# Kernel tuning notes

Measured on AMD Instinct MI355X. Metric: run time of the kernel, lower is better.

The kernel has to match this reference:

```python
import jax, jax.numpy as jnp
import numpy as np


def setup_inputs() -> dict:
    key = jax.random.key(0)
    ks = jax.random.split(key, 8)
    B, E, R, D, H = 8, 50000, 1000, 128, 256
    return {
        "head": jax.random.randint(ks[0], (B,), 0, E),
        "relation": jax.random.randint(ks[1], (B,), 0, R),
        "k": 10,
        "ent_emb": jax.random.normal(ks[2], (E, D), jnp.float32),
        "rel_emb": jax.random.normal(ks[3], (R, D), jnp.float32),
        "W1": jax.random.normal(ks[4], (3 * D, H), jnp.float32) * 0.05,
        "b1": jax.random.normal(ks[5], (H,), jnp.float32) * 0.05,
        "W2": jax.random.normal(ks[6], (H,), jnp.float32) * 0.05,
        "b2": jax.random.normal(ks[7], (1,), jnp.float32) * 0.05,
    }


def reference(head, relation, k, ent_emb, rel_emb, W1, b1, W2, b2):
    D = ent_emb.shape[1]
    # score_net first layer on cat([h, r, t]) == h@W1h + r@W1r + t@W1t (same math,
    # avoids materializing the [B*E, 3D] concat).
    W1h, W1r, W1t = W1[:D], W1[D:2 * D], W1[2 * D:]
    h = ent_emb[head]            # [B, D]
    r = rel_emb[relation]        # [B, D]
    ph = h @ W1h + r @ W1r + b1  # [B, H] -- head/relation part, computed once
    pt = ent_emb @ W1t           # [E, H] -- tail part over all entities
    hidden = jax.nn.relu(ph[:, None, :] + pt[None, :, :])   # [B, E, H]
    scores = jnp.einsum('beh,h->be', hidden, W2) + b2[0]     # [B, E]
    top_scores, top_indices = jax.lax.top_k(scores, k)
    return top_indices, top_scores
```

## Files before the change

kernel.cpp:

```cpp
#include <hip/hip_runtime.h>

#define D 128
#define HDIM 256
#define NB 8
#define NSHARD 32
#define CPS 16
#define LCPS 4
#define NCAND (NSHARD * CPS)
#define PHW 16
#define WPAD 136

typedef short bf16x8 __attribute__((ext_vector_type(8)));
typedef float f32x4 __attribute__((ext_vector_type(4)));

__device__ __forceinline__ unsigned short f2bf(float x) {
    unsigned u = __float_as_uint(x);
    unsigned r = u + 0x7FFF + ((u >> 16) & 1);
    return (unsigned short)(r >> 16);
}
__device__ __forceinline__ bf16x8 pack_bf8(float4 u, float4 v) {
    union { bf16x8 v8; unsigned short s[8]; } r;
    r.s[0] = f2bf(u.x); r.s[1] = f2bf(u.y); r.s[2] = f2bf(u.z); r.s[3] = f2bf(u.w);
    r.s[4] = f2bf(v.x); r.s[5] = f2bf(v.y); r.s[6] = f2bf(v.z); r.s[7] = f2bf(v.w);
    return r.v8;
}

__device__ __forceinline__ unsigned long long sk_encode(float v, int idx) {
    unsigned u = __float_as_uint(v);
    u = (u & 0x80000000u) ? ~u : (u | 0x80000000u);
    return ((unsigned long long)u << 32) | (unsigned)(0xFFFFFFFFu - (unsigned)idx);
}
__device__ __forceinline__ float sk_val(unsigned long long key) {
    const unsigned u = (unsigned)(key >> 32);
    return (u & 0x80000000u) ? __uint_as_float(u & 0x7FFFFFFFu) : __uint_as_float(~u);
}
__device__ __forceinline__ int sk_idx(unsigned long long key) {
    return (int)(0xFFFFFFFFu - (unsigned)(key & 0xFFFFFFFFu));
}
__device__ __forceinline__ unsigned long long wave_max64(unsigned long long m) {
#pragma unroll
    for (int s = 32; s > 0; s >>= 1) {
        const unsigned long long o = __shfl_xor(m, s, 64);
        if (o > m) m = o;
    }
    return m;
}

__global__ __launch_bounds__(1024) void prep_kernel(
        const int* __restrict__ head, const int* __restrict__ relation,
        const float* __restrict__ ent_emb, const float* __restrict__ rel_emb,
        const float* __restrict__ W1, const float* __restrict__ b1,
        const float* __restrict__ W2, float* __restrict__ phW,
        unsigned short* __restrict__ w1tt) {
    __shared__ float part[4][HDIM];
    const int w = blockIdx.x;
    const int tid = threadIdx.x;
    const int h = tid & 255;
    const int sl = tid >> 8;
    if (w < NB) {
        const int b = w;
        const long hidx = head[b];
        const long ridx = relation[b];
        const float* hrow = ent_emb + hidx * D;
        const float* rrow = rel_emb + ridx * D;
        float acc = 0.f;
        const int d0 = sl * 32;
#pragma unroll 8
        for (int dd = 0; dd < 32; ++dd) {
            const int d = d0 + dd;
            acc += hrow[d] * W1[d * HDIM + h];
            acc += rrow[d] * W1[(D + d) * HDIM + h];
        }
        part[sl][h] = acc;
        __syncthreads();
        if (sl == 0) {
            phW[h * PHW + b] = part[0][h] + part[1][h] + part[2][h] + part[3][h] + b1[h];
            if (b == 0) phW[h * PHW + 8] = W2[h];
        }
    } else {
        const int k0 = (w - NB) * 16 + sl * 4;
        const float* w1t = W1 + 2 * D * HDIM;
        unsigned short pk[4];
#pragma unroll
        for (int j = 0; j < 4; ++j)
            pk[j] = f2bf(w1t[(k0 + j) * HDIM + h]);
        *(ushort4*)(w1tt + h * D + k0) = make_ushort4(pk[0], pk[1], pk[2], pk[3]);
    }
}

__global__ __launch_bounds__(512, 2) void score_kernel(
        const float* __restrict__ ent_emb, const unsigned short* __restrict__ w1tt,
        const float* __restrict__ phW, float* __restrict__ scores, int E) {
    __shared__ __align__(16) unsigned short wL[HDIM][WPAD];
    __shared__ float phB[NB][HDIM];
    __shared__ float w2L[HDIM];

    const int tid = threadIdx.x;
    const int lane = tid & 63;
    const int wave = tid >> 6;
    const int lm = lane & 15;
    const int q = lane >> 4;
    const int base_e = blockIdx.x * 128 + wave * 16;

    const float* arow = ent_emb + (size_t)min(base_e + lm, E - 1) * D;
    bf16x8 aF[4];
#pragma unroll
    for (int kk = 0; kk < 4; ++kk) {
        const float4 u = *(const float4*)(arow + kk * 32 + q * 8);
        const float4 v = *(const float4*)(arow + kk * 32 + q * 8 + 4);
        aF[kk] = pack_bf8(u, v);
    }

#pragma unroll
    for (int i = 0; i < 8; ++i) {
        const int c = i * 512 + tid;
        const int row = c >> 4;
        const int col = (c & 15) << 3;
        *(uint4*)(&wL[row][col]) = *(const uint4*)(w1tt + row * D + col);
    }
    if (tid < HDIM) {
        const float4 p0 = *(const float4*)(phW + tid * PHW);
        const float4 p1 = *(const float4*)(phW + tid * PHW + 4);
        phB[0][tid] = -p0.x; phB[1][tid] = -p0.y; phB[2][tid] = -p0.z; phB[3][tid] = -p0.w;
        phB[4][tid] = -p1.x; phB[5][tid] = -p1.y; phB[6][tid] = -p1.z; phB[7][tid] = -p1.w;
        w2L[tid] = phW[tid * PHW + 8];
    }
    __syncthreads();

    float sp[NB * 4];
#pragma unroll
    for (int i = 0; i < NB * 4; ++i) sp[i] = 0.f;

#pragma unroll
    for (int t = 0; t < 16; ++t) {
        const int h = t * 16 + lm;
        bf16x8 bF[4];
#pragma unroll
        for (int kk = 0; kk < 4; ++kk)
            bF[kk] = *(const bf16x8*)(&wL[h][kk * 32 + q * 8]);

        float nphv[8];
#pragma unroll
        for (int b = 0; b < NB; ++b) nphv[b] = phB[b][h];
        const float w2v = w2L[h];

        f32x4 acc = (f32x4){0.f, 0.f, 0.f, 0.f};
#pragma unroll
        for (int kk = 0; kk < 4; ++kk)
            acc = __builtin_amdgcn_mfma_f32_16x16x32_bf16(aF[kk], bF[kk], acc, 0, 0, 0);

#pragma unroll
        for (int b = 0; b < NB; ++b)
#pragma unroll
            for (int r = 0; r < 4; ++r)
                sp[b * 4 + r] += fmaxf(acc[r], nphv[b]) * w2v;
    }

#pragma unroll
    for (int m = 1; m <= 8; m <<= 1) {
#pragma unroll
        for (int i = 0; i < NB * 4; ++i)
            sp[i] += __shfl_xor(sp[i], m, 64);
    }
    if (lm == 0) {
#pragma unroll
        for (int r = 0; r < 4; ++r) {
            const int e = base_e + q * 4 + r;
            if (e < E) {
#pragma unroll
                for (int b = 0; b < NB; ++b)
                    scores[(size_t)b * E + e] = sp[b * 4 + r];
            }
        }
    }
}

__global__ __launch_bounds__(512) void topk_rescore_kernel(
        const float* __restrict__ scores, int E,
        const float* __restrict__ ent_emb, const float* __restrict__ W1,
        const float* __restrict__ phW, const float* __restrict__ b2,
        unsigned long long* __restrict__ cand_exact) {
    const int b = blockIdx.x >> 5;
    const int s = blockIdx.x & 31;
    const int tid = threadIdx.x;
    const int lane = tid & 63;
    const int wave = tid >> 6;

    __shared__ unsigned long long cl[8 * CPS];
    __shared__ unsigned long long s2[32];
    __shared__ unsigned long long candk[CPS];
    __shared__ int eIdxs[CPS];
    __shared__ float entR[CPS][D];
    __shared__ float red[8][8];

    {
        const int shard = (E + NSHARD - 1) / NSHARD;
        const int start = s * shard;
        const int end = min(E, start + shard);
        const float* row = scores + (size_t)b * E;

        unsigned long long keys[LCPS];
#pragma unroll
        for (int i = 0; i < LCPS; ++i) keys[i] = 0ull;

        for (int e = start + tid; e < end; e += 512) {
            unsigned long long key = sk_encode(row[e], e);
            if (key > keys[LCPS - 1]) {
#pragma unroll
                for (int j = 0; j < LCPS; ++j) {
                    const bool gt = key > keys[j];
                    const unsigned long long mx = gt ? key : keys[j];
                    key = gt ? keys[j] : key;
                    keys[j] = mx;
                }
            }
        }
        for (int r = 0; r < CPS; ++r) {
            const unsigned long long m = wave_max64(keys[0]);
            if (keys[0] == m) {
#pragma unroll
                for (int j = 0; j < LCPS - 1; ++j) keys[j] = keys[j + 1];
                keys[LCPS - 1] = 0ull;
            }
            if (lane == 0) cl[wave * CPS + r] = m;
        }
        __syncthreads();
        if (wave < 2) {
            unsigned long long v = cl[wave * 64 + lane];
#pragma unroll
            for (int kk = 2; kk <= 64; kk <<= 1) {
#pragma unroll
                for (int j = kk >> 1; j > 0; j >>= 1) {
                    const unsigned long long o = __shfl_xor(v, j, 64);
                    const bool keep_min = (((lane & j) == 0) == ((lane & kk) != 0));
                    const unsigned long long mn = v < o ? v : o;
                    const unsigned long long mx = v < o ? o : v;
                    v = keep_min ? mn : mx;
                }
            }
            if (lane < 16) s2[wave * 16 + lane] = v;
        }
        __syncthreads();
        if (wave == 0) {
            unsigned long long v = 0ull;
            if (lane < 16) v = s2[lane];
            else if (lane < 32) v = s2[47 - lane];
#pragma unroll
            for (int j = 16; j > 0; j >>= 1) {
                const unsigned long long o = __shfl_xor(v, j, 64);
                const unsigned long long mn = v < o ? v : o;
                const unsigned long long mx = v < o ? o : v;
                v = ((lane & j) == 0) ? mx : mn;
            }
            if (lane < 16) candk[lane] = v;
        }
        __syncthreads();
    }

    if (tid < CPS) eIdxs[tid] = sk_idx(candk[tid]);
    __syncthreads();
    for (int t = tid; t < CPS * (D / 4); t += 512) {
        const int rowc = t >> 5, c4 = (t & 31) * 4;
        *(float4*)(&entR[rowc][c4]) =
            *(const float4*)(ent_emb + (size_t)eIdxs[rowc] * D + c4);
    }
    __syncthreads();

    const int h = tid & 255;
    const int chalf = tid >> 8;
    const float* w1t = W1 + 2 * D * HDIM;
    float acc[8];
#pragma unroll
    for (int c = 0; c < 8; ++c) acc[c] = 0.f;
    for (int d0 = 0; d0 < D; d0 += 4) {
        float w[4];
#pragma unroll
        for (int j = 0; j < 4; ++j) w[j] = w1t[(d0 + j) * HDIM + h];
#pragma unroll
        for (int c = 0; c < 8; ++c) {
            const float4 f = *(const float4*)(&entR[chalf * 8 + c][d0]);
            acc[c] += f.x * w[0] + f.y * w[1] + f.z * w[2] + f.w * w[3];
        }
    }
    const float phv = phW[h * PHW + b];
    const float w2v = phW[h * PHW + 8];
    float sc[8];
#pragma unroll
    for (int c = 0; c < 8; ++c) sc[c] = fmaxf(acc[c] + phv, 0.f) * w2v;

#pragma unroll
    for (int m = 1; m <= 32; m <<= 1)
#pragma unroll
        for (int c = 0; c < 8; ++c) sc[c] += __shfl_xor(sc[c], m, 64);
    if (lane == 0)
#pragma unroll
        for (int c = 0; c < 8; ++c) red[wave][c] = sc[c];
    __syncthreads();
    if (tid < CPS) {
        const int ch = tid >> 3, ci = tid & 7;
        const float v = red[ch * 4 + 0][ci] + red[ch * 4 + 1][ci] +
                        red[ch * 4 + 2][ci] + red[ch * 4 + 3][ci] + b2[0];
        cand_exact[(size_t)(b * NSHARD + s) * CPS + tid] = sk_encode(v, eIdxs[tid]);
    }
}

__global__ __launch_bounds__(64) void final_kernel(
        const unsigned long long* __restrict__ cand_exact, int k,
        float* __restrict__ out) {
    const int lane = threadIdx.x;
    const int b = blockIdx.x;
    unsigned long long lk[8];
#pragma unroll
    for (int j = 0; j < 8; ++j)
        lk[j] = cand_exact[(size_t)b * NCAND + j * 64 + lane];
#pragma unroll
    for (int i = 0; i < 7; ++i)
#pragma unroll
        for (int j = i + 1; j < 8; ++j)
            if (lk[i] < lk[j]) {
                const unsigned long long t = lk[i];
                lk[i] = lk[j];
                lk[j] = t;
            }
    for (int r = 0; r < k; ++r) {
        const unsigned long long m = wave_max64(lk[0]);
        if (lk[0] == m) {
#pragma unroll
            for (int j = 0; j < 7; ++j) lk[j] = lk[j + 1];
            lk[7] = 0ull;
        }
        if (lane == 0) {
            out[b * k + r] = (float)sk_idx(m);
            out[NB * k + b * k + r] = sk_val(m);
        }
    }
}

extern "C" void kernel_launch(void* const* d_in, const int* in_sizes, int n_in,
                              void* d_out, int out_size, void* d_ws, size_t ws_size,
                              hipStream_t stream) {
    const int*   head     = (const int*)d_in[0];
    const int*   relation = (const int*)d_in[1];
    const float* ent_emb  = (const float*)d_in[3];
    const float* rel_emb  = (const float*)d_in[4];
    const float* W1       = (const float*)d_in[5];
    const float* b1       = (const float*)d_in[6];
    const float* W2       = (const float*)d_in[7];
    const float* b2       = (const float*)d_in[8];

    const int B = in_sizes[0];
    const int E = in_sizes[3] / D;
    int k = out_size / (2 * B);
    if (k > CPS) k = CPS;

    char* ws = (char*)d_ws;
    unsigned long long* cand_exact = (unsigned long long*)ws;
    float*          phW       = (float*)(ws + 32768);
    unsigned short* w1tt      = (unsigned short*)(ws + 49152);
    float*          scores    = (float*)(ws + 114688);
    float*          out       = (float*)d_out;

    prep_kernel<<<NB + 8, 1024, 0, stream>>>(head, relation, ent_emb, rel_emb,
                                             W1, b1, W2, phW, w1tt);
    const int nblk = (E + 127) / 128;
    score_kernel<<<nblk, 512, 0, stream>>>(ent_emb, w1tt, phW, scores, E);
    topk_rescore_kernel<<<NB * NSHARD, 512, 0, stream>>>(
        scores, E, ent_emb, W1, phW, b2, cand_exact);
    final_kernel<<<NB, 64, 0, stream>>>(cand_exact, k, out);
}
```

Measured before the change: 133.1 us.

## Process two entity tiles per wave and use packed FMA epilogue in score kernel

The score kernel now runs 256 threads per block, with each wave handling 32 entities (two 16-row MFMA tiles) instead of 16. Each B fragment and phase value loaded from LDS is therefore reused across two tiles. The relu-times-W2 epilogue is rewritten with v_pk_fma_f32 and packed adds, and the per-h phase values and W2 are interleaved into one transposed LDS array so they load as vectors. This aims to cut LDS read traffic and VALU instruction count per entity, at the cost of more registers per thread and half as many threads per block.

After: 135.6 us. Within noise of the previous version (+1.9%).

```diff
diff --git a/kernel.cpp b/kernel.cpp
--- a/kernel.cpp
+++ b/kernel.cpp
@@ -9,9 +9,11 @@
 #define NCAND (NSHARD * CPS)
 #define PHW 16
 #define WPAD 136
+#define PHT 10
 
 typedef short bf16x8 __attribute__((ext_vector_type(8)));
 typedef float f32x4 __attribute__((ext_vector_type(4)));
+typedef float f32x2 __attribute__((ext_vector_type(2)));
 
 __device__ __forceinline__ unsigned short f2bf(float x) {
     unsigned u = __float_as_uint(x);
@@ -23,6 +25,16 @@
     r.s[0] = f2bf(u.x); r.s[1] = f2bf(u.y); r.s[2] = f2bf(u.z); r.s[3] = f2bf(u.w);
     r.s[4] = f2bf(v.x); r.s[5] = f2bf(v.y); r.s[6] = f2bf(v.z); r.s[7] = f2bf(v.w);
     return r.v8;
+}
+
+__device__ __forceinline__ f32x2 pk_fma(f32x2 a, f32x2 b, f32x2 c) {
+    asm("v_pk_fma_f32 %0, %1, %2, %0" : "+v"(c) : "v"(a), "v"(b));
+    return c;
+}
+__device__ __forceinline__ f32x2 pk_add(f32x2 a, f32x2 b) {
+    f32x2 d;
+    asm("v_pk_add_f32 %0, %1, %2" : "=v"(d) : "v"(a), "v"(b));
+    return d;
 }
 
 __device__ __forceinline__ unsigned long long sk_encode(float v, int idx) {
@@ -88,48 +100,52 @@
     }
 }
 
-__global__ __launch_bounds__(512, 2) void score_kernel(
+__global__ __launch_bounds__(256, 2) void score_kernel(
         const float* __restrict__ ent_emb, const unsigned short* __restrict__ w1tt,
         const float* __restrict__ phW, float* __restrict__ scores, int E) {
     __shared__ __align__(16) unsigned short wL[HDIM][WPAD];
-    __shared__ float phB[NB][HDIM];
-    __shared__ float w2L[HDIM];
+    __shared__ __align__(8) float phT[HDIM][PHT];
 
     const int tid = threadIdx.x;
     const int lane = tid & 63;
     const int wave = tid >> 6;
     const int lm = lane & 15;
     const int q = lane >> 4;
-    const int base_e = blockIdx.x * 128 + wave * 16;
-
-    const float* arow = ent_emb + (size_t)min(base_e + lm, E - 1) * D;
-    bf16x8 aF[4];
-#pragma unroll
-    for (int kk = 0; kk < 4; ++kk) {
-        const float4 u = *(const float4*)(arow + kk * 32 + q * 8);
-        const float4 v = *(const float4*)(arow + kk * 32 + q * 8 + 4);
-        aF[kk] = pack_bf8(u, v);
-    }
-
-#pragma unroll
-    for (int i = 0; i < 8; ++i) {
-        const int c = i * 512 + tid;
+    const int base_e = blockIdx.x * 128 + wave * 32;
+
+    bf16x8 aF[2][4];
+#pragma unroll
+    for (int tl = 0; tl < 2; ++tl) {
+        const float* arow = ent_emb + (size_t)min(base_e + tl * 16 + lm, E - 1) * D;
+#pragma unroll
+        for (int kk = 0; kk < 4; ++kk) {
+            const float4 u = *(const float4*)(arow + kk * 32 + q * 8);
+            const float4 v = *(const float4*)(arow + kk * 32 + q * 8 + 4);
+            aF[tl][kk] = pack_bf8(u, v);
+        }
+    }
+
+#pragma unroll
+    for (int i = 0; i < 16; ++i) {
+        const int c = i * 256 + tid;
         const int row = c >> 4;
         const int col = (c & 15) << 3;
         *(uint4*)(&wL[row][col]) = *(const uint4*)(w1tt + row * D + col);
     }
-    if (tid < HDIM) {
+    {
         const float4 p0 = *(const float4*)(phW + tid * PHW);
         const float4 p1 = *(const float4*)(phW + tid * PHW + 4);
-        phB[0][tid] = -p0.x; phB[1][tid] = -p0.y; phB[2][tid] = -p0.z; phB[3][tid] = -p0.w;
-        phB[4][tid] = -p1.x; phB[5][tid] = -p1.y; phB[6][tid] = -p1.z; phB[7][tid] = -p1.w;
-        w2L[tid] = phW[tid * PHW + 8];
+        phT[tid][0] = -p0.x; phT[tid][1] = -p0.y; phT[tid][2] = -p0.z; phT[tid][3] = -p0.w;
+        phT[tid][4] = -p1.x; phT[tid][5] = -p1.y; phT[tid][6] = -p1.z; phT[tid][7] = -p1.w;
+        phT[tid][8] = phW[tid * PHW + 8];
     }
     __syncthreads();
 
-    float sp[NB * 4];
-#pragma unroll
-    for (int i = 0; i < NB * 4; ++i) sp[i] = 0.f;
+    f32x2 sp[2][16];
+#pragma unroll
+    for (int tl = 0; tl < 2; ++tl)
+#pragma unroll
+        for (int i = 0; i < 16; ++i) sp[tl][i] = (f32x2){0.f, 0.f};
 
 #pragma unroll
     for (int t = 0; t < 16; ++t) {
@@ -139,39 +155,59 @@
         for (int kk = 0; kk < 4; ++kk)
             bF[kk] = *(const bf16x8*)(&wL[h][kk * 32 + q * 8]);
 
-        float nphv[8];
-#pragma unroll
-        for (int b = 0; b < NB; ++b) nphv[b] = phB[b][h];
-        const float w2v = w2L[h];
-
-        f32x4 acc = (f32x4){0.f, 0.f, 0.f, 0.f};
-#pragma unroll
-        for (int kk = 0; kk < 4; ++kk)
-            acc = __builtin_amdgcn_mfma_f32_16x16x32_bf16(aF[kk], bF[kk], acc, 0, 0, 0);
-
-#pragma unroll
-        for (int b = 0; b < NB; ++b)
-#pragma unroll
-            for (int r = 0; r < 4; ++r)
-                sp[b * 4 + r] += fmaxf(acc[r], nphv[b]) * w2v;
+        const float* ph = phT[h];
+        const f32x2 n01 = *(const f32x2*)(ph + 0);
+        const f32x2 n23 = *(const f32x2*)(ph + 2);
+        const f32x2 n45 = *(const f32x2*)(ph + 4);
+        const f32x2 n67 = *(const f32x2*)(ph + 6);
+        const float w2v = ph[8];
+        const f32x2 w2x2 = {w2v, w2v};
+        const float nph[8] = {n01.x, n01.y, n23.x, n23.y, n45.x, n45.y, n67.x, n67.y};
+
+#pragma unroll
+        for (int tl = 0; tl < 2; ++tl) {
+            f32x4 acc = (f32x4){0.f, 0.f, 0.f, 0.f};
+#pragma unroll
+            for (int kk = 0; kk < 4; ++kk)
+                acc = __builtin_amdgcn_mfma_f32_16x16x32_bf16(aF[tl][kk], bF[kk], acc, 0, 0, 0);
+
+#pragma unroll
+            for (int b = 0; b < NB; ++b) {
+                const float nb = nph[b];
+                const f32x2 m0 = {fmaxf(acc[0], nb), fmaxf(acc[1], nb)};
+                sp[tl][b * 2 + 0] = pk_fma(m0, w2x2, sp[tl][b * 2 + 0]);
+                const f32x2 m1 = {fmaxf(acc[2], nb), fmaxf(acc[3], nb)};
+                sp[tl][b * 2 + 1] = pk_fma(m1, w2x2, sp[tl][b * 2 + 1]);
+            }
+        }
     }
 
 #pragma unroll
     for (int m = 1; m <= 8; m <<= 1) {
 #pragma unroll
-        for (int i = 0; i < NB * 4; ++i)
-            sp[i] += __shfl_xor(sp[i], m, 64);
+        for (int tl = 0; tl < 2; ++tl)
+#pragma unroll
+            for (int i = 0; i < 16; ++i) {
+                union { f32x2 f; unsigned long long u; } cv;
+                cv.f = sp[tl][i];
+                cv.u = __shfl_xor(cv.u, m, 64);
+                sp[tl][i] = pk_add(sp[tl][i], cv.f);
+            }
     }
     if (lm == 0) {
 #pragma unroll
-        for (int r = 0; r < 4; ++r) {
-            const int e = base_e + q * 4 + r;
-            if (e < E) {
-#pragma unroll
-                for (int b = 0; b < NB; ++b)
-                    scores[(size_t)b * E + e] = sp[b * 4 + r];
-            }
-        }
+        for (int tl = 0; tl < 2; ++tl)
+#pragma unroll
+            for (int rp = 0; rp < 2; ++rp)
+#pragma unroll
+                for (int j = 0; j < 2; ++j) {
+                    const int e = base_e + tl * 16 + q * 4 + rp * 2 + j;
+                    if (e < E) {
+#pragma unroll
+                        for (int b = 0; b < NB; ++b)
+                            scores[(size_t)b * E + e] = sp[tl][b * 2 + rp][j];
+                    }
+                }
     }
 }
 
@@ -363,7 +399,7 @@
     prep_kernel<<<NB + 8, 1024, 0, stream>>>(head, relation, ent_emb, rel_emb,
                                              W1, b1, W2, phW, w1tt);
     const int nblk = (E + 127) / 128;
-    score_kernel<<<nblk, 512, 0, stream>>>(ent_emb, w1tt, phW, scores, E);
+    score_kernel<<<nblk, 256, 0, stream>>>(ent_emb, w1tt, phW, scores, E);
     topk_rescore_kernel<<<NB * NSHARD, 512, 0, stream>>>(
         scores, E, ent_emb, W1, phW, b2, cand_exact);
     final_kernel<<<NB, 64, 0, stream>>>(cand_exact, k, out);
```
